# Optimization experiments

Hardware: AMD Instinct MI355X
Metric: run time of the kernel (lower is better)

Reference implementation:

```python
import jax, jax.numpy as jnp
import numpy as np

D_MODEL = 1024
D_FEATURE = 64
N_HEADS = D_MODEL // D_FEATURE  # 16


def setup_inputs() -> dict:
    key = jax.random.key(0)
    ks = jax.random.split(key, 11)
    B, S = 2, 2048
    s = 1.0 / np.sqrt(D_MODEL)
    inp = {
        "queries": jax.random.normal(ks[0], (B, S, D_MODEL), dtype=jnp.float32),
        "keys": jax.random.normal(ks[1], (B, S, D_MODEL), dtype=jnp.float32),
        "values": jax.random.normal(ks[2], (B, S, D_MODEL), dtype=jnp.float32),
        # Per-head Q/K/V projection weights stacked over heads: [H, d_model, d_feature]
        "Wq": jax.random.normal(ks[3], (N_HEADS, D_MODEL, D_FEATURE), dtype=jnp.float32) * s,
        "Wk": jax.random.normal(ks[4], (N_HEADS, D_MODEL, D_FEATURE), dtype=jnp.float32) * s,
        "Wv": jax.random.normal(ks[5], (N_HEADS, D_MODEL, D_FEATURE), dtype=jnp.float32) * s,
        "bq": jax.random.normal(ks[6], (N_HEADS, D_FEATURE), dtype=jnp.float32) * 0.01,
        "bk": jax.random.normal(ks[7], (N_HEADS, D_FEATURE), dtype=jnp.float32) * 0.01,
        "bv": jax.random.normal(ks[8], (N_HEADS, D_FEATURE), dtype=jnp.float32) * 0.01,
        # Output projection Linear(d_model, d_model)
        "Wo": jax.random.normal(ks[9], (D_MODEL, D_MODEL), dtype=jnp.float32) * s,
        "bo": jax.random.normal(ks[10], (D_MODEL,), dtype=jnp.float32) * 0.01,
    }
    return inp


def reference(queries, keys, values, Wq, Wk, Wv, bq, bk, bv, Wo, bo):
    # Batched equivalent of the per-head loop: all heads' Q/K/V projections
    # done as single einsums, fused multi-head scaled-dot-product attention,
    # then concat (reshape) + output projection. Dropout is identity (eval).
    scale = 1.0 / jnp.sqrt(jnp.asarray(D_FEATURE, queries.dtype))
    q = jnp.einsum("bsd,hdf->bhsf", queries, Wq) + bq[None, :, None, :]
    k = jnp.einsum("bsd,hdf->bhsf", keys, Wk) + bk[None, :, None, :]
    v = jnp.einsum("bsd,hdf->bhsf", values, Wv) + bv[None, :, None, :]
    scores = jnp.einsum("bhsf,bhtf->bhst", q, k) * scale  # [B,H,S,S]
    attn = jax.nn.softmax(scores, axis=-1)
    out = jnp.einsum("bhst,bhtf->bhsf", attn, v)  # [B,H,S,F]
    B, H, S, F = out.shape
    # torch.cat(heads, dim=2): head outputs laid out contiguously -> (h f)
    out = out.transpose(0, 2, 1, 3).reshape(B, S, H * F)
    return out @ Wo.T + bo  # final Linear(d_model, d_model)
```

## Files before the change

kernel.cpp:

```cpp
#include <hip/hip_runtime.h>
#include <hip/hip_bf16.h>

typedef __bf16 bf16_t;
typedef __bf16 bf16x4 __attribute__((ext_vector_type(4)));
typedef __bf16 bf16x8 __attribute__((ext_vector_type(8)));
typedef _Float16 f16_t;
typedef _Float16 f16x4 __attribute__((ext_vector_type(4)));
typedef _Float16 f16x8 __attribute__((ext_vector_type(8)));
typedef __fp16 hf2 __attribute__((ext_vector_type(2)));
typedef float f32x4 __attribute__((ext_vector_type(4)));

#define MFMA16(a, b, c)  __builtin_amdgcn_mfma_f32_16x16x32_bf16((a), (b), (c), 0, 0, 0)
#define MFMA32H(a, b, c) __builtin_amdgcn_mfma_f32_16x16x32_f16((a), (b), (c), 0, 0, 0)

#define QSCALE 0.18033688089869237f

typedef __attribute__((address_space(3))) void lds_void;
typedef const __attribute__((address_space(1))) void glob_void;
static __device__ __forceinline__ void gl_lds16(const void* g, void* l) {
    __builtin_amdgcn_global_load_lds((glob_void*)g, (lds_void*)l, 16, 0, 0);
}

__global__ __launch_bounds__(256) void prep(
    const float* __restrict__ Wq, const float* __restrict__ Wk,
    const float* __restrict__ Wv, const float* __restrict__ Wo,
    const float* __restrict__ qin, const float* __restrict__ kin,
    const float* __restrict__ vin,
    bf16_t* __restrict__ WqT, bf16_t* __restrict__ WkT,
    bf16_t* __restrict__ WvT, bf16_t* __restrict__ WoT,
    bf16_t* __restrict__ qb, bf16_t* __restrict__ kb, bf16_t* __restrict__ vb)
{
    const int t = threadIdx.x;
    if (blockIdx.x < 256) {
        __shared__ float tile[64][65];
        const int h = blockIdx.x >> 4, d0 = (blockIdx.x & 15) << 6;
        const float* Ws[3] = {Wq, Wk, Wv};
        bf16_t* Wt[3] = {WqT, WkT, WvT};
        const int r = t >> 4, c4 = (t & 15) << 2;
        for (int s = 0; s < 3; ++s) {
            const float* W = Ws[s] + ((size_t)h << 16);
#pragma unroll
            for (int i = 0; i < 4; ++i) {
                float4 v = *(const float4*)&W[(size_t)(d0 + i * 16 + r) * 64 + c4];
                tile[i * 16 + r][c4 + 0] = v.x; tile[i * 16 + r][c4 + 1] = v.y;
                tile[i * 16 + r][c4 + 2] = v.z; tile[i * 16 + r][c4 + 3] = v.w;
            }
            __syncthreads();
#pragma unroll
            for (int i = 0; i < 4; ++i) {
                int f = i * 16 + r;
                bf16x4 o;
                o[0] = (bf16_t)tile[c4 + 0][f]; o[1] = (bf16_t)tile[c4 + 1][f];
                o[2] = (bf16_t)tile[c4 + 2][f]; o[3] = (bf16_t)tile[c4 + 3][f];
                *(bf16x4*)&Wt[s][(((size_t)(h << 6) + f) << 10) + d0 + c4] = o;
            }
            __syncthreads();
        }
    } else {
        size_t id = (size_t)(blockIdx.x - 256) * 256 + t;
        size_t e = id * 4;
        {
            float4 v = *(const float4*)&qin[e];
            bf16x4 o = {(bf16_t)v.x, (bf16_t)v.y, (bf16_t)v.z, (bf16_t)v.w};
            *(bf16x4*)&qb[e] = o;
        }
        {
            float4 v = *(const float4*)&kin[e];
            bf16x4 o = {(bf16_t)v.x, (bf16_t)v.y, (bf16_t)v.z, (bf16_t)v.w};
            *(bf16x4*)&kb[e] = o;
        }
        {
            float4 v = *(const float4*)&vin[e];
            bf16x4 o = {(bf16_t)v.x, (bf16_t)v.y, (bf16_t)v.z, (bf16_t)v.w};
            *(bf16x4*)&vb[e] = o;
        }
        if (id < 262144) {
            float4 v = *(const float4*)&Wo[e];
            bf16x4 o = {(bf16_t)v.x, (bf16_t)v.y, (bf16_t)v.z, (bf16_t)v.w};
            *(bf16x4*)&WoT[e] = o;
        }
    }
}

static __device__ __forceinline__ void gemm_core128(
    const bf16_t* __restrict__ A, const bf16_t* __restrict__ B,
    int m0, int n0, bf16_t* As, bf16_t* Bs, f32x4 acc[4][4])
{
    const int tid = threadIdx.x, lane = tid & 63, w = tid >> 6;
    const int m = lane & 15, quad = lane >> 4;
    const int wm = (w >> 1) * 64, wn = (w & 1) * 64;
    const int lrow = lane >> 3;
    const int lcol = (((lane & 7) ^ (lrow & 7)) << 3);

    for (int kt = 0; kt < 1024; kt += 64) {
#pragma unroll
        for (int i = 0; i < 4; ++i) {
            int chunk = i * 4 + w;
            int row = chunk * 8 + lrow;
            gl_lds16(A + (size_t)(m0 + row) * 1024 + kt + lcol, As + chunk * 512);
            gl_lds16(B + (size_t)(n0 + row) * 1024 + kt + lcol, Bs + chunk * 512);
        }
        __syncthreads();
#pragma unroll
        for (int kc = 0; kc < 2; ++kc) {
            bf16x8 af[4], bfr[4];
#pragma unroll
            for (int x = 0; x < 4; ++x) {
                int ra = wm + x * 16 + m, rb = wn + x * 16 + m;
                int co = ((kc * 4 + quad) ^ (m & 7)) << 3;
                af[x]  = *(const bf16x8*)&As[ra * 64 + co];
                bfr[x] = *(const bf16x8*)&Bs[rb * 64 + co];
            }
#pragma unroll
            for (int mt = 0; mt < 4; ++mt)
#pragma unroll
                for (int nt = 0; nt < 4; ++nt)
                    acc[mt][nt] = MFMA16(af[mt], bfr[nt], acc[mt][nt]);
        }
        __syncthreads();
    }
}

__global__ __launch_bounds__(256) void gemm_proj(
    const bf16_t* __restrict__ qb, const bf16_t* __restrict__ kb,
    const bf16_t* __restrict__ vb, const bf16_t* __restrict__ WT,
    const float* __restrict__ bq, const float* __restrict__ bk,
    const float* __restrict__ bv,
    bf16_t* __restrict__ Qs, bf16_t* __restrict__ Ksb, f16_t* __restrict__ Vt)
{
    __shared__ alignas(16) bf16_t As[8192], Bs[8192];
    const int id = blockIdx.x;
    const int z = id >> 8, rem = id & 255;
    const int n0 = (rem >> 5) * 128, m0 = (rem & 31) * 128;
    const bf16_t* A = (z == 0) ? qb : (z == 1) ? kb : vb;
    const bf16_t* B = WT + (size_t)z * (1024 * 1024);
    const float* bias = (z == 0) ? bq : (z == 1) ? bk : bv;

    f32x4 zero = {0.f, 0.f, 0.f, 0.f};
    f32x4 acc[4][4];
#pragma unroll
    for (int i = 0; i < 4; ++i)
#pragma unroll
        for (int j = 0; j < 4; ++j) acc[i][j] = zero;

    gemm_core128(A, B, m0, n0, As, Bs, acc);

    const int lane = threadIdx.x & 63, w = threadIdx.x >> 6;
    const int m = lane & 15, quad = lane >> 4;
    const int wm = (w >> 1) * 64, wn = (w & 1) * 64;

    if (z == 2) {
#pragma unroll
        for (int mt = 0; mt < 4; ++mt)
#pragma unroll
            for (int nt = 0; nt < 4; ++nt) {
                int col = n0 + wn + nt * 16 + m;
                float bb = bias[col];
                int row0 = m0 + wm + mt * 16 + quad * 4;
                int bi = row0 >> 11, s = row0 & 2047;
                f16x4 p;
#pragma unroll
                for (int r = 0; r < 4; ++r) p[r] = (f16_t)(acc[mt][nt][r] + bb);
                *(f16x4*)&Vt[((size_t)bi * 1024 + col) * 2048 + s] = p;
            }
    } else {
        bf16_t* out = z ? Ksb : Qs;
        float sc = z ? 1.0f : QSCALE;
#pragma unroll
        for (int mt = 0; mt < 4; ++mt)
#pragma unroll
            for (int nt = 0; nt < 4; ++nt) {
                int col = n0 + wn + nt * 16 + m;
                float bb = bias[col];
#pragma unroll
                for (int r = 0; r < 4; ++r) {
                    int row = m0 + wm + mt * 16 + quad * 4 + r;
                    out[(size_t)row * 1024 + col] = (bf16_t)((acc[mt][nt][r] + bb) * sc);
                }
            }
    }
}

__global__ __launch_bounds__(256) void gemm_out(
    const bf16_t* __restrict__ Aos, const bf16_t* __restrict__ WoT,
    const float* __restrict__ bo, float* __restrict__ out)
{
    __shared__ alignas(16) bf16_t As[128 * 64], Bs[64 * 64];
    const int tid = threadIdx.x, lane = tid & 63, w = tid >> 6;
    const int m = lane & 15, quad = lane >> 4;
    const int wm = (w >> 1) * 64, wn = (w & 1) * 32;
    const int id = blockIdx.x;
    const int m0 = (id & 31) * 128, n0 = (id >> 5) * 64;
    const int lrow = lane >> 3;
    const int lcol = (((lane & 7) ^ (lrow & 7)) << 3);

    f32x4 zero = {0.f, 0.f, 0.f, 0.f};
    f32x4 acc[4][2];
#pragma unroll
    for (int i = 0; i < 4; ++i) { acc[i][0] = zero; acc[i][1] = zero; }

    for (int kt = 0; kt < 1024; kt += 64) {
#pragma unroll
        for (int i = 0; i < 4; ++i) {
            int chunk = i * 4 + w;
            gl_lds16(Aos + (size_t)(m0 + chunk * 8 + lrow) * 1024 + kt + lcol, As + chunk * 512);
        }
#pragma unroll
        for (int i = 0; i < 2; ++i) {
            int chunk = i * 4 + w;
            gl_lds16(WoT + (size_t)(n0 + chunk * 8 + lrow) * 1024 + kt + lcol, Bs + chunk * 512);
        }
        __syncthreads();
#pragma unroll
        for (int kc = 0; kc < 2; ++kc) {
            bf16x8 af[4], bfr[2];
#pragma unroll
            for (int x = 0; x < 4; ++x) {
                int row = wm + x * 16 + m;
                af[x] = *(const bf16x8*)&As[row * 64 + (((kc * 4 + quad) ^ (m & 7)) << 3)];
            }
#pragma unroll
            for (int x = 0; x < 2; ++x) {
                int row = wn + x * 16 + m;
                bfr[x] = *(const bf16x8*)&Bs[row * 64 + (((kc * 4 + quad) ^ (m & 7)) << 3)];
            }
#pragma unroll
            for (int mt = 0; mt < 4; ++mt)
#pragma unroll
                for (int nt = 0; nt < 2; ++nt)
                    acc[mt][nt] = MFMA16(af[mt], bfr[nt], acc[mt][nt]);
        }
        __syncthreads();
    }

#pragma unroll
    for (int mt = 0; mt < 4; ++mt)
#pragma unroll
        for (int nt = 0; nt < 2; ++nt) {
            int col = n0 + wn + nt * 16 + m;
            float bb = bo[col];
#pragma unroll
            for (int r = 0; r < 4; ++r) {
                int row = m0 + wm + mt * 16 + quad * 4 + r;
                out[(size_t)row * 1024 + col] = acc[mt][nt][r] + bb;
            }
        }
}

__global__ __launch_bounds__(256, 4) void attn5(
    const bf16_t* __restrict__ Qb, const bf16_t* __restrict__ Kb,
    const f16_t* __restrict__ Vt, f16_t* __restrict__ Op, float* __restrict__ Ls)
{
    __shared__ alignas(16) bf16_t Ks[2][32][72];
    __shared__ alignas(16) f16_t  Vts[2][64][40];

    const int tid = threadIdx.x, lane = tid & 63, w = tid >> 6;
    const int m = lane & 15, quad = lane >> 4;
    const int bh = blockIdx.x, b = bh >> 4, h = bh & 15;
    const int q0 = blockIdx.y * 128;
    const int ks = blockIdx.z;
    const int kt0 = ks << 10;
    const size_t base = (size_t)b * 2048 * 1024 + h * 64;
    const size_t vbase = ((size_t)b * 1024 + h * 64) * 2048;

    bf16x8 aq[2][2];
#pragma unroll
    for (int qt = 0; qt < 2; ++qt) {
        const bf16_t* qp = Qb + base + (size_t)(q0 + w * 32 + qt * 16 + m) * 1024;
        aq[qt][0] = *(const bf16x8*)(qp + quad * 8);
        aq[qt][1] = *(const bf16x8*)(qp + 32 + quad * 8);
    }
    f16x8 ones8;
#pragma unroll
    for (int j = 0; j < 8; ++j) ones8[j] = (f16_t)1.0f;

    f32x4 zero = {0.f, 0.f, 0.f, 0.f};
    f32x4 acc[2][5];
#pragma unroll
    for (int qt = 0; qt < 2; ++qt)
#pragma unroll
        for (int i = 0; i < 5; ++i) acc[qt][i] = zero;

    const int kkey = tid >> 3, kfo = (tid & 7) * 8;
    const int vf = tid >> 2, vko = (tid & 3) * 8;

    bf16x8 rk = *(const bf16x8*)(Kb + base + (size_t)(kt0 + kkey) * 1024 + kfo);
    f16x8  rv = *(const f16x8*)(Vt + vbase + (size_t)vf * 2048 + kt0 + vko);

    int buf = 0;
    for (int kt = kt0; kt < kt0 + 1024; kt += 32) {
        *(bf16x8*)&Ks[buf][kkey][kfo] = rk;
        *(f16x8*)&Vts[buf][vf][vko] = rv;
        __syncthreads();
        if (kt + 32 < kt0 + 1024) {
            rk = *(const bf16x8*)(Kb + base + (size_t)(kt + 32 + kkey) * 1024 + kfo);
            rv = *(const f16x8*)(Vt + vbase + (size_t)vf * 2048 + kt + 32 + vko);
        }

        f32x4 s[2][2];
#pragma unroll
        for (int kl = 0; kl < 2; ++kl) {
            bf16x8 a0 = *(const bf16x8*)&Ks[buf][kl * 16 + m][quad * 8];
            bf16x8 a1 = *(const bf16x8*)&Ks[buf][kl * 16 + m][32 + quad * 8];
#pragma unroll
            for (int qt = 0; qt < 2; ++qt) {
                f32x4 t = MFMA16(a0, aq[qt][0], zero);
                s[kl][qt] = MFMA16(a1, aq[qt][1], t);
            }
        }

        f16x8 p[2];
#pragma unroll
        for (int qt = 0; qt < 2; ++qt)
#pragma unroll
            for (int kl = 0; kl < 2; ++kl) {
                hf2 lo = __builtin_amdgcn_cvt_pkrtz(
                    __builtin_amdgcn_exp2f(s[kl][qt][0]),
                    __builtin_amdgcn_exp2f(s[kl][qt][1]));
                hf2 hi = __builtin_amdgcn_cvt_pkrtz(
                    __builtin_amdgcn_exp2f(s[kl][qt][2]),
                    __builtin_amdgcn_exp2f(s[kl][qt][3]));
                p[qt][kl * 4 + 0] = lo[0]; p[qt][kl * 4 + 1] = lo[1];
                p[qt][kl * 4 + 2] = hi[0]; p[qt][kl * 4 + 3] = hi[1];
            }

#pragma unroll
        for (int ft = 0; ft < 4; ++ft) {
            f16x4 lo = *(const f16x4*)&Vts[buf][ft * 16 + m][quad * 4];
            f16x4 hi = *(const f16x4*)&Vts[buf][ft * 16 + m][16 + quad * 4];
            f16x8 bv;
#pragma unroll
            for (int j = 0; j < 4; ++j) { bv[j] = lo[j]; bv[4 + j] = hi[j]; }
#pragma unroll
            for (int qt = 0; qt < 2; ++qt)
                acc[qt][ft] = MFMA32H(p[qt], bv, acc[qt][ft]);
        }
#pragma unroll
        for (int qt = 0; qt < 2; ++qt)
            acc[qt][4] = MFMA32H(p[qt], ones8, acc[qt][4]);

        buf ^= 1;
    }

#pragma unroll
    for (int qt = 0; qt < 2; ++qt)
#pragma unroll
        for (int r = 0; r < 4; ++r) {
            int grow = (b << 11) + q0 + w * 32 + qt * 16 + quad * 4 + r;
            f16_t* op = Op + (((size_t)ks << 12) + grow) * 1024 + (h << 6);
#pragma unroll
            for (int ft = 0; ft < 4; ++ft)
                op[ft * 16 + m] = (f16_t)(acc[qt][ft][r]);
            if (m == 0)
                Ls[((((size_t)ks << 12) + grow) << 4) + h] = acc[qt][4][r];
        }
}

__global__ __launch_bounds__(256) void combine(
    const f16_t* __restrict__ Op, const float* __restrict__ Ls,
    bf16_t* __restrict__ Os)
{
    size_t idx = ((size_t)blockIdx.x * 256 + threadIdx.x) * 8;
    int row = (int)(idx >> 10), h = (int)((idx & 1023) >> 6);
    f16x8 a = *(const f16x8*)&Op[idx];
    f16x8 c = *(const f16x8*)&Op[(size_t)4096 * 1024 + idx];
    float l = Ls[row * 16 + h] + Ls[4096 * 16 + row * 16 + h];
    float inv = __builtin_amdgcn_rcpf(l);
    bf16x8 o;
#pragma unroll
    for (int i = 0; i < 8; ++i)
        o[i] = (bf16_t)(((float)a[i] + (float)c[i]) * inv);
    *(bf16x8*)&Os[idx] = o;
}

extern "C" void kernel_launch(void* const* d_in, const int* in_sizes, int n_in,
                              void* d_out, int out_size, void* d_ws, size_t ws_size,
                              hipStream_t stream)
{
    const float* queries = (const float*)d_in[0];
    const float* keys    = (const float*)d_in[1];
    const float* values  = (const float*)d_in[2];
    const float* Wq = (const float*)d_in[3];
    const float* Wk = (const float*)d_in[4];
    const float* Wv = (const float*)d_in[5];
    const float* bq = (const float*)d_in[6];
    const float* bk = (const float*)d_in[7];
    const float* bv = (const float*)d_in[8];
    const float* Wo = (const float*)d_in[9];
    const float* bo = (const float*)d_in[10];

    char* ws = (char*)d_ws;
    const size_t MB = 1024 * 1024;
    bf16_t* WqT = (bf16_t*)(ws + 0 * MB);
    bf16_t* WkT = (bf16_t*)(ws + 2 * MB);
    bf16_t* WvT = (bf16_t*)(ws + 4 * MB);
    bf16_t* WoT = (bf16_t*)(ws + 6 * MB);
    bf16_t* qb  = (bf16_t*)(ws + 8 * MB);
    bf16_t* kb  = (bf16_t*)(ws + 16 * MB);
    bf16_t* vb  = (bf16_t*)(ws + 24 * MB);
    f16_t*  Vt  = (f16_t*)(ws + 32 * MB);
    f16_t*  Op  = (f16_t*)(ws + 40 * MB);
    float*  Lsp = (float*)(ws + 56 * MB);
    bf16_t* Qs  = (bf16_t*)d_out;
    bf16_t* Ksb = (bf16_t*)((char*)d_out + 8 * MB);
    bf16_t* Os  = qb;
    (void)WkT; (void)WvT;

    prep<<<4352, 256, 0, stream>>>(Wq, Wk, Wv, Wo, queries, keys, values,
                                   WqT, WkT, WvT, WoT, qb, kb, vb);

    gemm_proj<<<768, 256, 0, stream>>>(qb, kb, vb, WqT, bq, bk, bv,
                                       Qs, Ksb, Vt);

    attn5<<<dim3(32, 16, 2), 256, 0, stream>>>(Qs, Ksb, Vt, Op, Lsp);

    combine<<<2048, 256, 0, stream>>>(Op, Lsp, Os);

    gemm_out<<<512, 256, 0, stream>>>(Os, WoT, bo, (float*)d_out);
}
```

Baseline: 225.7 us.

## Fuse split-K combine into output GEMM and shrink projection GEMM tiles

Removes the separate combine kernel and moves its work into the output GEMM. The output GEMM now reads both f16 partial outputs and their softmax denominators, normalizes them, converts to bf16 and writes the result into LDS, which saves a launch and a global round trip through the intermediate. The projection GEMM moves from 128x128 to 128x64 tiles with twice as many blocks and a launch-bounds occupancy hint of 6. The output GEMM moves to 64x64 tiles. In exchange, the A operand of the output GEMM is loaded synchronously through registers and is no longer an async LDS load, and the smaller tiles give less data reuse per block.

```diff
diff --git a/kernel.cpp b/kernel.cpp
--- a/kernel.cpp
+++ b/kernel.cpp
@@ -82,13 +82,13 @@
     }
 }
 
-static __device__ __forceinline__ void gemm_core128(
+static __device__ __forceinline__ void gemm_core64(
     const bf16_t* __restrict__ A, const bf16_t* __restrict__ B,
-    int m0, int n0, bf16_t* As, bf16_t* Bs, f32x4 acc[4][4])
+    int m0, int n0, bf16_t* As, bf16_t* Bs, f32x4 acc[4][2])
 {
     const int tid = threadIdx.x, lane = tid & 63, w = tid >> 6;
     const int m = lane & 15, quad = lane >> 4;
-    const int wm = (w >> 1) * 64, wn = (w & 1) * 64;
+    const int wm = (w >> 1) * 64, wn = (w & 1) * 32;
     const int lrow = lane >> 3;
     const int lcol = (((lane & 7) ^ (lrow & 7)) << 3);
 
@@ -96,64 +96,68 @@
 #pragma unroll
         for (int i = 0; i < 4; ++i) {
             int chunk = i * 4 + w;
-            int row = chunk * 8 + lrow;
-            gl_lds16(A + (size_t)(m0 + row) * 1024 + kt + lcol, As + chunk * 512);
-            gl_lds16(B + (size_t)(n0 + row) * 1024 + kt + lcol, Bs + chunk * 512);
+            gl_lds16(A + (size_t)(m0 + chunk * 8 + lrow) * 1024 + kt + lcol, As + chunk * 512);
+        }
+#pragma unroll
+        for (int i = 0; i < 2; ++i) {
+            int chunk = i * 4 + w;
+            gl_lds16(B + (size_t)(n0 + chunk * 8 + lrow) * 1024 + kt + lcol, Bs + chunk * 512);
         }
         __syncthreads();
 #pragma unroll
         for (int kc = 0; kc < 2; ++kc) {
-            bf16x8 af[4], bfr[4];
+            bf16x8 af[4], bfr[2];
 #pragma unroll
             for (int x = 0; x < 4; ++x) {
-                int ra = wm + x * 16 + m, rb = wn + x * 16 + m;
-                int co = ((kc * 4 + quad) ^ (m & 7)) << 3;
-                af[x]  = *(const bf16x8*)&As[ra * 64 + co];
-                bfr[x] = *(const bf16x8*)&Bs[rb * 64 + co];
+                int row = wm + x * 16 + m;
+                af[x] = *(const bf16x8*)&As[row * 64 + (((kc * 4 + quad) ^ (m & 7)) << 3)];
+            }
+#pragma unroll
+            for (int x = 0; x < 2; ++x) {
+                int row = wn + x * 16 + m;
+                bfr[x] = *(const bf16x8*)&Bs[row * 64 + (((kc * 4 + quad) ^ (m & 7)) << 3)];
             }
 #pragma unroll
             for (int mt = 0; mt < 4; ++mt)
 #pragma unroll
-                for (int nt = 0; nt < 4; ++nt)
+                for (int nt = 0; nt < 2; ++nt)
                     acc[mt][nt] = MFMA16(af[mt], bfr[nt], acc[mt][nt]);
         }
         __syncthreads();
     }
 }
 
-__global__ __launch_bounds__(256) void gemm_proj(
+__global__ __launch_bounds__(256, 6) void gemm_proj(
     const bf16_t* __restrict__ qb, const bf16_t* __restrict__ kb,
     const bf16_t* __restrict__ vb, const bf16_t* __restrict__ WT,
     const float* __restrict__ bq, const float* __restrict__ bk,
     const float* __restrict__ bv,
     bf16_t* __restrict__ Qs, bf16_t* __restrict__ Ksb, f16_t* __restrict__ Vt)
 {
-    __shared__ alignas(16) bf16_t As[8192], Bs[8192];
+    __shared__ alignas(16) bf16_t As[128 * 64], Bs[64 * 64];
     const int id = blockIdx.x;
-    const int z = id >> 8, rem = id & 255;
-    const int n0 = (rem >> 5) * 128, m0 = (rem & 31) * 128;
+    const int z = id >> 9, rem = id & 511;
+    const int n0 = (rem >> 5) * 64, m0 = (rem & 31) * 128;
     const bf16_t* A = (z == 0) ? qb : (z == 1) ? kb : vb;
     const bf16_t* B = WT + (size_t)z * (1024 * 1024);
     const float* bias = (z == 0) ? bq : (z == 1) ? bk : bv;
 
     f32x4 zero = {0.f, 0.f, 0.f, 0.f};
-    f32x4 acc[4][4];
-#pragma unroll
-    for (int i = 0; i < 4; ++i)
-#pragma unroll
-        for (int j = 0; j < 4; ++j) acc[i][j] = zero;
-
-    gemm_core128(A, B, m0, n0, As, Bs, acc);
+    f32x4 acc[4][2];
+#pragma unroll
+    for (int i = 0; i < 4; ++i) { acc[i][0] = zero; acc[i][1] = zero; }
+
+    gemm_core64(A, B, m0, n0, As, Bs, acc);
 
     const int lane = threadIdx.x & 63, w = threadIdx.x >> 6;
     const int m = lane & 15, quad = lane >> 4;
-    const int wm = (w >> 1) * 64, wn = (w & 1) * 64;
+    const int wm = (w >> 1) * 64, wn = (w & 1) * 32;
 
     if (z == 2) {
 #pragma unroll
         for (int mt = 0; mt < 4; ++mt)
 #pragma unroll
-            for (int nt = 0; nt < 4; ++nt) {
+            for (int nt = 0; nt < 2; ++nt) {
                 int col = n0 + wn + nt * 16 + m;
                 float bb = bias[col];
                 int row0 = m0 + wm + mt * 16 + quad * 4;
@@ -169,7 +173,7 @@
 #pragma unroll
         for (int mt = 0; mt < 4; ++mt)
 #pragma unroll
-            for (int nt = 0; nt < 4; ++nt) {
+            for (int nt = 0; nt < 2; ++nt) {
                 int col = n0 + wn + nt * 16 + m;
                 float bb = bias[col];
 #pragma unroll
@@ -181,51 +185,59 @@
     }
 }
 
-__global__ __launch_bounds__(256) void gemm_out(
-    const bf16_t* __restrict__ Aos, const bf16_t* __restrict__ WoT,
-    const float* __restrict__ bo, float* __restrict__ out)
-{
-    __shared__ alignas(16) bf16_t As[128 * 64], Bs[64 * 64];
+__global__ __launch_bounds__(256, 4) void gemm_out_fused(
+    const f16_t* __restrict__ Op, const float* __restrict__ Ls,
+    const bf16_t* __restrict__ WoT, const float* __restrict__ bo,
+    float* __restrict__ out)
+{
+    __shared__ alignas(16) bf16_t As[64 * 64], Bs[64 * 64];
     const int tid = threadIdx.x, lane = tid & 63, w = tid >> 6;
     const int m = lane & 15, quad = lane >> 4;
-    const int wm = (w >> 1) * 64, wn = (w & 1) * 32;
+    const int wm = (w >> 1) * 32, wn = (w & 1) * 32;
     const int id = blockIdx.x;
-    const int m0 = (id & 31) * 128, n0 = (id >> 5) * 64;
+    const int m0 = (id & 63) * 64, n0 = (id >> 6) * 64;
     const int lrow = lane >> 3;
     const int lcol = (((lane & 7) ^ (lrow & 7)) << 3);
+    const int arow = tid >> 3, acol = (tid & 7) * 8;
 
     f32x4 zero = {0.f, 0.f, 0.f, 0.f};
-    f32x4 acc[4][2];
-#pragma unroll
-    for (int i = 0; i < 4; ++i) { acc[i][0] = zero; acc[i][1] = zero; }
+    f32x4 acc[2][2];
+    acc[0][0] = zero; acc[0][1] = zero; acc[1][0] = zero; acc[1][1] = zero;
 
     for (int kt = 0; kt < 1024; kt += 64) {
-#pragma unroll
-        for (int i = 0; i < 4; ++i) {
-            int chunk = i * 4 + w;
-            gl_lds16(Aos + (size_t)(m0 + chunk * 8 + lrow) * 1024 + kt + lcol, As + chunk * 512);
-        }
+        const int h = kt >> 6;
 #pragma unroll
         for (int i = 0; i < 2; ++i) {
             int chunk = i * 4 + w;
             gl_lds16(WoT + (size_t)(n0 + chunk * 8 + lrow) * 1024 + kt + lcol, Bs + chunk * 512);
         }
+#pragma unroll
+        for (int p = 0; p < 2; ++p) {
+            int row = p * 32 + arow;
+            int grow = m0 + row;
+            f16x8 a0 = *(const f16x8*)&Op[(size_t)grow * 1024 + kt + acol];
+            f16x8 a1 = *(const f16x8*)&Op[(size_t)(4096 + grow) * 1024 + kt + acol];
+            float l = Ls[grow * 16 + h] + Ls[(4096 + grow) * 16 + h];
+            float inv = __builtin_amdgcn_rcpf(l);
+            bf16x8 av;
+#pragma unroll
+            for (int j = 0; j < 8; ++j)
+                av[j] = (bf16_t)(((float)a0[j] + (float)a1[j]) * inv);
+            *(bf16x8*)&As[row * 64 + ((((tid & 7) ^ (row & 7))) << 3)] = av;
+        }
         __syncthreads();
 #pragma unroll
         for (int kc = 0; kc < 2; ++kc) {
-            bf16x8 af[4], bfr[2];
-#pragma unroll
-            for (int x = 0; x < 4; ++x) {
-                int row = wm + x * 16 + m;
-                af[x] = *(const bf16x8*)&As[row * 64 + (((kc * 4 + quad) ^ (m & 7)) << 3)];
-            }
+            bf16x8 af[2], bfr[2];
 #pragma unroll
             for (int x = 0; x < 2; ++x) {
-                int row = wn + x * 16 + m;
-                bfr[x] = *(const bf16x8*)&Bs[row * 64 + (((kc * 4 + quad) ^ (m & 7)) << 3)];
-            }
-#pragma unroll
-            for (int mt = 0; mt < 4; ++mt)
+                int ra = wm + x * 16 + m, rb = wn + x * 16 + m;
+                int co = ((kc * 4 + quad) ^ (m & 7)) << 3;
+                af[x]  = *(const bf16x8*)&As[ra * 64 + co];
+                bfr[x] = *(const bf16x8*)&Bs[rb * 64 + co];
+            }
+#pragma unroll
+            for (int mt = 0; mt < 2; ++mt)
 #pragma unroll
                 for (int nt = 0; nt < 2; ++nt)
                     acc[mt][nt] = MFMA16(af[mt], bfr[nt], acc[mt][nt]);
@@ -234,7 +246,7 @@
     }
 
 #pragma unroll
-    for (int mt = 0; mt < 4; ++mt)
+    for (int mt = 0; mt < 2; ++mt)
 #pragma unroll
         for (int nt = 0; nt < 2; ++nt) {
             int col = n0 + wn + nt * 16 + m;
@@ -354,23 +366,6 @@
             if (m == 0)
                 Ls[((((size_t)ks << 12) + grow) << 4) + h] = acc[qt][4][r];
         }
-}
-
-__global__ __launch_bounds__(256) void combine(
-    const f16_t* __restrict__ Op, const float* __restrict__ Ls,
-    bf16_t* __restrict__ Os)
-{
-    size_t idx = ((size_t)blockIdx.x * 256 + threadIdx.x) * 8;
-    int row = (int)(idx >> 10), h = (int)((idx & 1023) >> 6);
-    f16x8 a = *(const f16x8*)&Op[idx];
-    f16x8 c = *(const f16x8*)&Op[(size_t)4096 * 1024 + idx];
-    float l = Ls[row * 16 + h] + Ls[4096 * 16 + row * 16 + h];
-    float inv = __builtin_amdgcn_rcpf(l);
-    bf16x8 o;
-#pragma unroll
-    for (int i = 0; i < 8; ++i)
-        o[i] = (bf16_t)(((float)a[i] + (float)c[i]) * inv);
-    *(bf16x8*)&Os[idx] = o;
 }
 
 extern "C" void kernel_launch(void* const* d_in, const int* in_sizes, int n_in,
@@ -403,18 +398,15 @@
     float*  Lsp = (float*)(ws + 56 * MB);
     bf16_t* Qs  = (bf16_t*)d_out;
     bf16_t* Ksb = (bf16_t*)((char*)d_out + 8 * MB);
-    bf16_t* Os  = qb;
     (void)WkT; (void)WvT;
 
     prep<<<4352, 256, 0, stream>>>(Wq, Wk, Wv, Wo, queries, keys, values,
                                    WqT, WkT, WvT, WoT, qb, kb, vb);
 
-    gemm_proj<<<768, 256, 0, stream>>>(qb, kb, vb, WqT, bq, bk, bv,
-                                       Qs, Ksb, Vt);
+    gemm_proj<<<1536, 256, 0, stream>>>(qb, kb, vb, WqT, bq, bk, bv,
+                                        Qs, Ksb, Vt);
 
     attn5<<<dim3(32, 16, 2), 256, 0, stream>>>(Qs, Ksb, Vt, Op, Lsp);
 
-    combine<<<2048, 256, 0, stream>>>(Op, Lsp, Os);
-
-    gemm_out<<<512, 256, 0, stream>>>(Os, WoT, bo, (float*)d_out);
-}
+    gemm_out_fused<<<1024, 256, 0, stream>>>(Op, Lsp, WoT, bo, (float*)d_out);
+}
```

After: 244.7 us. +8.4%, slower.
